# Performance work log

Hardware: AMD Instinct MI355X
Metric: run time of the kernel (lower is better)

Reference implementation:

```python
import jax, jax.numpy as jnp
import numpy as np

N_NODES = 100_000   # number of nodes
N_EDGES = 1_600_000 # number of edges (avg degree 16)
D_IN    = 64        # node feature dim
E_W     = 16        # edge feature ('w') dim -> message dim D_IN + E_W
EPS     = 0.0       # init_eps, non-learnable buffer


def setup_inputs() -> dict:
    key = jax.random.key(0)
    k1, k2, k3, k4, k5 = jax.random.split(key, 5)
    feat = jax.random.normal(k1, (N_NODES, D_IN), dtype=jnp.float32)
    edge_w = jax.random.normal(k2, (N_EDGES, E_W), dtype=jnp.float32)
    src = jax.random.randint(k3, (N_EDGES,), 0, N_NODES)
    dst = jax.random.randint(k4, (N_EDGES,), 0, N_NODES)
    # apply_func: Linear(D_IN + E_W -> D_IN)
    W = jax.random.normal(k5, (D_IN + E_W, D_IN), dtype=jnp.float32) / np.float32(np.sqrt(D_IN + E_W))
    b = jnp.zeros((D_IN,), dtype=jnp.float32)
    return {"feat": feat, "edge_w": edge_w, "W": W, "b": b, "src": src, "dst": dst}


def reference(feat, edge_w, W, b, src, dst):
    n = feat.shape[0]
    # message m_e = concat(h[src_e], w_e); sum-aggregate over incoming edges of dst.
    # Sum of concat == concat of sums, avoiding materializing [E, D_IN+E_W].
    neigh_h = jax.ops.segment_sum(feat[src], dst, num_segments=n)     # [N, D_IN]
    neigh_w = jax.ops.segment_sum(edge_w, dst, num_segments=n)        # [N, E_W]
    neigh = jnp.concatenate([neigh_h, neigh_w], axis=-1)              # [N, D_IN+E_W]
    # pad feat with zeros to match widened message dim (as in the torch code)
    feat_pad = jnp.concatenate(
        [feat, jnp.zeros((n, neigh.shape[-1] - feat.shape[-1]), feat.dtype)], axis=-1
    )
    rst = (1.0 + EPS) * feat_pad + neigh                              # eps-residual
    rst = rst @ W + b                                                 # apply_func (Linear)
    return jax.nn.relu(rst)                                           # activation
```

## Files before the change

kernel.cpp:

```cpp
#include <hip/hip_runtime.h>

#define D_IN  64
#define E_W   16
#define D_MSG 80
#define NXCD  8

static __device__ __forceinline__ void f4add(float4& a, const float4& b) {
    a.x += b.x; a.y += b.y; a.z += b.z; a.w += b.w;
}

__global__ __launch_bounds__(256) void k_hist_sh(const int4* __restrict__ dst4,
                                                 const int* __restrict__ dst,
                                                 int* __restrict__ deg,
                                                 int E, int rng)
{
    int shard = blockIdx.x & (NXCD - 1);
    int wg    = blockIdx.x / NXCD;
    int lo    = shard * rng;
    int hi    = lo + rng;
    int E4    = E >> 2;

    int base = wg * 512;
    int stop = min(base + 512, E4);
    for (int i = base + threadIdx.x; i < stop; i += 256) {
        int4 d = dst4[i];
        if (d.x >= lo && d.x < hi) atomicAdd(deg + d.x, 1);
        if (d.y >= lo && d.y < hi) atomicAdd(deg + d.y, 1);
        if (d.z >= lo && d.z < hi) atomicAdd(deg + d.z, 1);
        if (d.w >= lo && d.w < hi) atomicAdd(deg + d.w, 1);
    }
    if (wg == 0 && threadIdx.x < (E & 3)) {
        int e = (E & ~3) + threadIdx.x;
        int d = dst[e];
        if (d >= lo && d < hi) atomicAdd(deg + d, 1);
    }
}

__global__ __launch_bounds__(256) void k_scan1(const int* __restrict__ deg,
                                               int* __restrict__ excl,
                                               int* __restrict__ bsums, int n)
{
    __shared__ int ts[256];
    int base = blockIdx.x * 1024 + threadIdx.x * 4;
    int v[4], s = 0;
    #pragma unroll
    for (int i = 0; i < 4; ++i) { v[i] = (base + i < n) ? deg[base + i] : 0; s += v[i]; }
    ts[threadIdx.x] = s; __syncthreads();
    #pragma unroll
    for (int off = 1; off < 256; off <<= 1) {
        int t = (threadIdx.x >= off) ? ts[threadIdx.x - off] : 0;
        __syncthreads();
        ts[threadIdx.x] += t;
        __syncthreads();
    }
    int run = ts[threadIdx.x] - s;
    if (threadIdx.x == 255) bsums[blockIdx.x] = ts[255];
    #pragma unroll
    for (int i = 0; i < 4; ++i) {
        if (base + i < n) excl[base + i] = run;
        run += v[i];
    }
}

__global__ __launch_bounds__(256) void k_scan2(int* __restrict__ bsums,
                                               int* __restrict__ bexcl, int nb)
{
    __shared__ int ts[256];
    int v = (threadIdx.x < nb) ? bsums[threadIdx.x] : 0;
    ts[threadIdx.x] = v; __syncthreads();
    #pragma unroll
    for (int off = 1; off < 256; off <<= 1) {
        int t = (threadIdx.x >= off) ? ts[threadIdx.x - off] : 0;
        __syncthreads();
        ts[threadIdx.x] += t;
        __syncthreads();
    }
    bexcl[threadIdx.x] = ts[threadIdx.x] - v;
}

__global__ __launch_bounds__(256) void k_scan3(const int* __restrict__ excl,
                                               const int* __restrict__ bexcl,
                                               int* __restrict__ offsets,
                                               int* __restrict__ cursor, int n, int E)
{
    int i = blockIdx.x * 256 + threadIdx.x;
    if (i < n) {
        int s = excl[i] + bexcl[i >> 10];
        offsets[i] = s;
        cursor[i]  = s;
    }
    if (i == 0) offsets[n] = E;
}

__global__ __launch_bounds__(256) void k_reorder_sh(const int4* __restrict__ src4,
                                                    const int4* __restrict__ dst4,
                                                    const int* __restrict__ src,
                                                    const int* __restrict__ dst,
                                                    int* __restrict__ cursor,
                                                    int2* __restrict__ sorted,
                                                    int E, int rng)
{
    int shard = blockIdx.x & (NXCD - 1);
    int wg    = blockIdx.x / NXCD;
    int lo    = shard * rng;
    int hi    = lo + rng;
    int E4    = E >> 2;

    int base = wg * 512;
    int stop = min(base + 512, E4);
    for (int i = base + threadIdx.x; i < stop; i += 256) {
        int4 d = dst4[i];
        bool any = (d.x >= lo && d.x < hi) | (d.y >= lo && d.y < hi) |
                   (d.z >= lo && d.z < hi) | (d.w >= lo && d.w < hi);
        if (!any) continue;
        int4 s = src4[i];
        int e = i * 4;
        if (d.x >= lo && d.x < hi) sorted[atomicAdd(cursor + d.x, 1)] = make_int2(s.x, e + 0);
        if (d.y >= lo && d.y < hi) sorted[atomicAdd(cursor + d.y, 1)] = make_int2(s.y, e + 1);
        if (d.z >= lo && d.z < hi) sorted[atomicAdd(cursor + d.z, 1)] = make_int2(s.z, e + 2);
        if (d.w >= lo && d.w < hi) sorted[atomicAdd(cursor + d.w, 1)] = make_int2(s.w, e + 3);
    }
    if (wg == 0 && threadIdx.x < (E & 3)) {
        int e = (E & ~3) + threadIdx.x;
        int d = dst[e];
        if (d >= lo && d < hi) sorted[atomicAdd(cursor + d, 1)] = make_int2(src[e], e);
    }
}

__global__ __launch_bounds__(256) void k_pull(const float4* __restrict__ feat4,
                                              const float4* __restrict__ ew4,
                                              const int2* __restrict__ sorted,
                                              const int* __restrict__ offsets,
                                              float4* __restrict__ acc_h4,
                                              float4* __restrict__ acc_w4, int N)
{
    int t = blockIdx.x * 256 + threadIdx.x;
    int node = t >> 4;
    if (node >= N) return;
    int l = t & 15;

    int beg = offsets[node];
    int end = offsets[node + 1];

    float4 ah = feat4[(size_t)node * 16 + l];
    float4 aw = make_float4(0.f, 0.f, 0.f, 0.f);

    int p = beg;
    for (; p + 4 <= end; p += 4) {
        int2 r0 = sorted[p + 0];
        int2 r1 = sorted[p + 1];
        int2 r2 = sorted[p + 2];
        int2 r3 = sorted[p + 3];
        float4 f0 = feat4[(size_t)r0.x * 16 + l];
        float4 f1 = feat4[(size_t)r1.x * 16 + l];
        float4 f2 = feat4[(size_t)r2.x * 16 + l];
        float4 f3 = feat4[(size_t)r3.x * 16 + l];
        if (l < 4) {
            float4 w0 = ew4[(size_t)r0.y * 4 + l];
            float4 w1 = ew4[(size_t)r1.y * 4 + l];
            float4 w2 = ew4[(size_t)r2.y * 4 + l];
            float4 w3 = ew4[(size_t)r3.y * 4 + l];
            f4add(aw, w0); f4add(aw, w1); f4add(aw, w2); f4add(aw, w3);
        }
        f4add(ah, f0); f4add(ah, f1); f4add(ah, f2); f4add(ah, f3);
    }
    for (; p < end; ++p) {
        int2 r = sorted[p];
        f4add(ah, feat4[(size_t)r.x * 16 + l]);
        if (l < 4) f4add(aw, ew4[(size_t)r.y * 4 + l]);
    }

    acc_h4[(size_t)node * 16 + l] = ah;
    if (l < 4) acc_w4[(size_t)node * 4 + l] = aw;
}

__global__ __launch_bounds__(256) void scatter_kernel(
    const float4* __restrict__ feat4, const float4* __restrict__ ew4,
    const int* __restrict__ src, const int* __restrict__ dst,
    float* __restrict__ acc_h, float* __restrict__ acc_w, int E)
{
    int t = blockIdx.x * 256 + threadIdx.x;
    int e = t >> 4;
    if (e >= E) return;
    int l = t & 15;
    int s = src[e];
    int d = dst[e];
    float4 hv = feat4[(size_t)s * 16 + l];
    float4 wv;
    bool do_w = (l < 4);
    if (do_w) wv = ew4[(size_t)e * 4 + l];
    float* p = acc_h + (size_t)d * D_IN + l * 4;
    unsafeAtomicAdd(p + 0, hv.x);
    unsafeAtomicAdd(p + 1, hv.y);
    unsafeAtomicAdd(p + 2, hv.z);
    unsafeAtomicAdd(p + 3, hv.w);
    if (do_w) {
        float* q = acc_w + (size_t)d * E_W + l * 4;
        unsafeAtomicAdd(q + 0, wv.x);
        unsafeAtomicAdd(q + 1, wv.y);
        unsafeAtomicAdd(q + 2, wv.z);
        unsafeAtomicAdd(q + 3, wv.w);
    }
}

__global__ __launch_bounds__(256) void gemm_relu_kernel(
    const float* __restrict__ feat, const float* __restrict__ acc_w,
    const float* __restrict__ Wm, const float* __restrict__ bias,
    float* __restrict__ out, int N, int add_feat)
{
    __shared__ float4 Wl[D_MSG * 16];
    __shared__ float4 bl4[16];
    __shared__ float  xs[64 * 84];

    for (int i = threadIdx.x; i < D_MSG * 16; i += 256)
        Wl[i] = ((const float4*)Wm)[i];
    if (threadIdx.x < 16)
        bl4[threadIdx.x] = ((const float4*)bias)[threadIdx.x];

    const int tc   = threadIdx.x & 15;
    const int tg   = threadIdx.x >> 4;
    const int base = blockIdx.x * 64;

    for (int i = threadIdx.x; i < 64 * 20; i += 256) {
        int r = i / 20, c = i % 20;
        int row = base + r;
        float4 v = make_float4(0.f, 0.f, 0.f, 0.f);
        if (row < N) {
            if (c < 16) {
                v = ((const float4*)out)[(size_t)row * 16 + c];
                if (add_feat) {
                    float4 f = ((const float4*)feat)[(size_t)row * 16 + c];
                    f4add(v, f);
                }
            } else {
                v = ((const float4*)acc_w)[(size_t)row * 4 + (c - 16)];
            }
        }
        *((float4*)&xs[r * 84 + c * 4]) = v;
    }
    __syncthreads();

    float4 ob = bl4[tc];
    float4 acc[4];
    acc[0] = ob; acc[1] = ob; acc[2] = ob; acc[3] = ob;

    #pragma unroll 4
    for (int k = 0; k < D_MSG; ++k) {
        float4 w = Wl[k * 16 + tc];
        #pragma unroll
        for (int rr = 0; rr < 4; ++rr) {
            float xk = xs[(tg * 4 + rr) * 84 + k];
            acc[rr].x += xk * w.x;
            acc[rr].y += xk * w.y;
            acc[rr].z += xk * w.z;
            acc[rr].w += xk * w.w;
        }
    }

    #pragma unroll
    for (int rr = 0; rr < 4; ++rr) {
        int row = base + tg * 4 + rr;
        if (row < N) {
            float4 v = acc[rr];
            v.x = fmaxf(v.x, 0.f);
            v.y = fmaxf(v.y, 0.f);
            v.z = fmaxf(v.z, 0.f);
            v.w = fmaxf(v.w, 0.f);
            ((float4*)out)[(size_t)row * 16 + tc] = v;
        }
    }
}

static inline size_t align256(size_t x) { return (x + 255) & ~(size_t)255; }

extern "C" void kernel_launch(void* const* d_in, const int* in_sizes, int n_in,
                              void* d_out, int out_size, void* d_ws, size_t ws_size,
                              hipStream_t stream) {
    const float* feat   = (const float*)d_in[0];
    const float* edge_w = (const float*)d_in[1];
    const float* Wm     = (const float*)d_in[2];
    const float* bias   = (const float*)d_in[3];
    const int*   src    = (const int*)d_in[4];
    const int*   dst    = (const int*)d_in[5];
    float* out = (float*)d_out;

    const int N = in_sizes[0] / D_IN;
    const int E = in_sizes[4];

    size_t o_accw   = 0;
    size_t o_deg    = align256(o_accw + (size_t)N * E_W * 4);
    size_t o_excl   = align256(o_deg  + (size_t)(N + 1) * 4);
    size_t o_off    = align256(o_excl + (size_t)N * 4);
    size_t o_cur    = align256(o_off  + (size_t)(N + 1) * 4);
    size_t o_bsum   = align256(o_cur  + (size_t)N * 4);
    size_t o_bexcl  = align256(o_bsum + 256 * 4);
    size_t o_sorted = align256(o_bexcl + 256 * 4);
    size_t need     = o_sorted + (size_t)E * 8;

    char* ws = (char*)d_ws;
    float* acc_w = (float*)(ws + o_accw);

    int used_fallback = 0;

    if (ws_size >= need) {
        int*  deg     = (int*) (ws + o_deg);
        int*  excl    = (int*) (ws + o_excl);
        int*  offsets = (int*) (ws + o_off);
        int*  cursor  = (int*) (ws + o_cur);
        int*  bsums   = (int*) (ws + o_bsum);
        int*  bexcl   = (int*) (ws + o_bexcl);
        int2* sorted  = (int2*)(ws + o_sorted);

        hipMemsetAsync(deg, 0, (size_t)(N + 1) * 4, stream);

        const int rng = (N + NXCD - 1) / NXCD;
        const int E4  = E >> 2;
        const int wg_per_shard = (E4 + 511) / 512;
        const int grid_sh = wg_per_shard * NXCD;

        k_hist_sh<<<grid_sh, 256, 0, stream>>>((const int4*)dst, dst, deg, E, rng);

        int nb1 = (N + 1023) / 1024;
        k_scan1<<<nb1, 256, 0, stream>>>(deg, excl, bsums, N);
        k_scan2<<<1, 256, 0, stream>>>(bsums, bexcl, nb1);
        k_scan3<<<(N + 255) / 256, 256, 0, stream>>>(excl, bexcl, offsets, cursor, N, E);

        k_reorder_sh<<<grid_sh, 256, 0, stream>>>(
            (const int4*)src, (const int4*)dst, src, dst, cursor, sorted, E, rng);

        k_pull<<<(N * 16 + 255) / 256, 256, 0, stream>>>(
            (const float4*)feat, (const float4*)edge_w, sorted, offsets,
            (float4*)out, (float4*)acc_w, N);
    } else {
        used_fallback = 1;
        hipMemsetAsync(d_out, 0, (size_t)N * D_IN * sizeof(float), stream);
        hipMemsetAsync(acc_w, 0, (size_t)N * E_W * sizeof(float), stream);
        long long tot = (long long)E * 16;
        scatter_kernel<<<(int)((tot + 255) / 256), 256, 0, stream>>>(
            (const float4*)feat, (const float4*)edge_w, src, dst, out, acc_w, E);
    }

    gemm_relu_kernel<<<(N + 63) / 64, 256, 0, stream>>>(
        feat, acc_w, Wm, bias, out, N, used_fallback);
}
```

Measured before the change: 417.4 us.

## Fuse pull aggregation with linear+ReLU and collapse scan into one kernel

Each block now aggregates neighbor features for 16 nodes into shared memory, then applies the 80x64 linear layer, bias and ReLU directly. This drops the separate GEMM kernel and the round trip of aggregated rows through global memory. The three-kernel prefix scan becomes a single 1024-thread block that scans 100K degrees serially per thread, which cuts launches but leaves that step on one CU. Every block also reloads W (20KB) into LDS, which adds load traffic and LDS pressure.

```diff
diff --git a/kernel.cpp b/kernel.cpp
--- a/kernel.cpp
+++ b/kernel.cpp
@@ -36,60 +36,35 @@
     }
 }
 
-__global__ __launch_bounds__(256) void k_scan1(const int* __restrict__ deg,
-                                               int* __restrict__ excl,
-                                               int* __restrict__ bsums, int n)
-{
-    __shared__ int ts[256];
-    int base = blockIdx.x * 1024 + threadIdx.x * 4;
-    int v[4], s = 0;
+__global__ __launch_bounds__(1024) void k_scan_one(const int* __restrict__ deg,
+                                                   int* __restrict__ offsets,
+                                                   int* __restrict__ cursor,
+                                                   int n, int E)
+{
+    __shared__ int ts[1024];
+    const int C = (n + 1023) / 1024;
+    int t  = threadIdx.x;
+    int lo = t * C;
+    int hi = min(lo + C, n);
+
+    int s = 0;
+    for (int i = lo; i < hi; ++i) s += deg[i];
+    ts[t] = s; __syncthreads();
     #pragma unroll
-    for (int i = 0; i < 4; ++i) { v[i] = (base + i < n) ? deg[base + i] : 0; s += v[i]; }
-    ts[threadIdx.x] = s; __syncthreads();
-    #pragma unroll
-    for (int off = 1; off < 256; off <<= 1) {
-        int t = (threadIdx.x >= off) ? ts[threadIdx.x - off] : 0;
+    for (int off = 1; off < 1024; off <<= 1) {
+        int v = (t >= off) ? ts[t - off] : 0;
         __syncthreads();
-        ts[threadIdx.x] += t;
+        ts[t] += v;
         __syncthreads();
     }
-    int run = ts[threadIdx.x] - s;
-    if (threadIdx.x == 255) bsums[blockIdx.x] = ts[255];
-    #pragma unroll
-    for (int i = 0; i < 4; ++i) {
-        if (base + i < n) excl[base + i] = run;
-        run += v[i];
-    }
-}
-
-__global__ __launch_bounds__(256) void k_scan2(int* __restrict__ bsums,
-                                               int* __restrict__ bexcl, int nb)
-{
-    __shared__ int ts[256];
-    int v = (threadIdx.x < nb) ? bsums[threadIdx.x] : 0;
-    ts[threadIdx.x] = v; __syncthreads();
-    #pragma unroll
-    for (int off = 1; off < 256; off <<= 1) {
-        int t = (threadIdx.x >= off) ? ts[threadIdx.x - off] : 0;
-        __syncthreads();
-        ts[threadIdx.x] += t;
-        __syncthreads();
-    }
-    bexcl[threadIdx.x] = ts[threadIdx.x] - v;
-}
-
-__global__ __launch_bounds__(256) void k_scan3(const int* __restrict__ excl,
-                                               const int* __restrict__ bexcl,
-                                               int* __restrict__ offsets,
-                                               int* __restrict__ cursor, int n, int E)
-{
-    int i = blockIdx.x * 256 + threadIdx.x;
-    if (i < n) {
-        int s = excl[i] + bexcl[i >> 10];
-        offsets[i] = s;
-        cursor[i]  = s;
-    }
-    if (i == 0) offsets[n] = E;
+    int run = ts[t] - s;
+    for (int i = lo; i < hi; ++i) {
+        int d = deg[i];
+        offsets[i] = run;
+        cursor[i]  = run;
+        run += d;
+    }
+    if (t == 0) offsets[n] = E;
 }
 
 __global__ __launch_bounds__(256) void k_reorder_sh(const int4* __restrict__ src4,
@@ -127,51 +102,81 @@
     }
 }
 
-__global__ __launch_bounds__(256) void k_pull(const float4* __restrict__ feat4,
-                                              const float4* __restrict__ ew4,
-                                              const int2* __restrict__ sorted,
-                                              const int* __restrict__ offsets,
-                                              float4* __restrict__ acc_h4,
-                                              float4* __restrict__ acc_w4, int N)
-{
-    int t = blockIdx.x * 256 + threadIdx.x;
-    int node = t >> 4;
-    if (node >= N) return;
-    int l = t & 15;
-
-    int beg = offsets[node];
-    int end = offsets[node + 1];
-
-    float4 ah = feat4[(size_t)node * 16 + l];
-    float4 aw = make_float4(0.f, 0.f, 0.f, 0.f);
-
-    int p = beg;
-    for (; p + 4 <= end; p += 4) {
-        int2 r0 = sorted[p + 0];
-        int2 r1 = sorted[p + 1];
-        int2 r2 = sorted[p + 2];
-        int2 r3 = sorted[p + 3];
-        float4 f0 = feat4[(size_t)r0.x * 16 + l];
-        float4 f1 = feat4[(size_t)r1.x * 16 + l];
-        float4 f2 = feat4[(size_t)r2.x * 16 + l];
-        float4 f3 = feat4[(size_t)r3.x * 16 + l];
-        if (l < 4) {
-            float4 w0 = ew4[(size_t)r0.y * 4 + l];
-            float4 w1 = ew4[(size_t)r1.y * 4 + l];
-            float4 w2 = ew4[(size_t)r2.y * 4 + l];
-            float4 w3 = ew4[(size_t)r3.y * 4 + l];
-            f4add(aw, w0); f4add(aw, w1); f4add(aw, w2); f4add(aw, w3);
-        }
-        f4add(ah, f0); f4add(ah, f1); f4add(ah, f2); f4add(ah, f3);
-    }
-    for (; p < end; ++p) {
-        int2 r = sorted[p];
-        f4add(ah, feat4[(size_t)r.x * 16 + l]);
-        if (l < 4) f4add(aw, ew4[(size_t)r.y * 4 + l]);
-    }
-
-    acc_h4[(size_t)node * 16 + l] = ah;
-    if (l < 4) acc_w4[(size_t)node * 4 + l] = aw;
+__global__ __launch_bounds__(256) void k_pull_gemm(const float4* __restrict__ feat4,
+                                                   const float4* __restrict__ ew4,
+                                                   const int2* __restrict__ sorted,
+                                                   const int* __restrict__ offsets,
+                                                   const float* __restrict__ Wm,
+                                                   const float* __restrict__ bias,
+                                                   float4* __restrict__ out4, int N)
+{
+    __shared__ float4 Wl[D_MSG * 16];
+    __shared__ float4 bl4[16];
+    __shared__ float  xs[16 * 84];
+
+    for (int i = threadIdx.x; i < D_MSG * 16; i += 256)
+        Wl[i] = ((const float4*)Wm)[i];
+    if (threadIdx.x < 16)
+        bl4[threadIdx.x] = ((const float4*)bias)[threadIdx.x];
+
+    const int nl   = threadIdx.x >> 4;
+    const int l    = threadIdx.x & 15;
+    const int node = blockIdx.x * 16 + nl;
+
+    if (node < N) {
+        int beg = offsets[node];
+        int end = offsets[node + 1];
+
+        float4 ah = feat4[(size_t)node * 16 + l];
+        float4 aw = make_float4(0.f, 0.f, 0.f, 0.f);
+
+        int p = beg;
+        for (; p + 4 <= end; p += 4) {
+            int2 r0 = sorted[p + 0];
+            int2 r1 = sorted[p + 1];
+            int2 r2 = sorted[p + 2];
+            int2 r3 = sorted[p + 3];
+            float4 f0 = feat4[(size_t)r0.x * 16 + l];
+            float4 f1 = feat4[(size_t)r1.x * 16 + l];
+            float4 f2 = feat4[(size_t)r2.x * 16 + l];
+            float4 f3 = feat4[(size_t)r3.x * 16 + l];
+            if (l < 4) {
+                float4 w0 = ew4[(size_t)r0.y * 4 + l];
+                float4 w1 = ew4[(size_t)r1.y * 4 + l];
+                float4 w2 = ew4[(size_t)r2.y * 4 + l];
+                float4 w3 = ew4[(size_t)r3.y * 4 + l];
+                f4add(aw, w0); f4add(aw, w1); f4add(aw, w2); f4add(aw, w3);
+            }
+            f4add(ah, f0); f4add(ah, f1); f4add(ah, f2); f4add(ah, f3);
+        }
+        for (; p < end; ++p) {
+            int2 r = sorted[p];
+            f4add(ah, feat4[(size_t)r.x * 16 + l]);
+            if (l < 4) f4add(aw, ew4[(size_t)r.y * 4 + l]);
+        }
+
+        *(float4*)&xs[nl * 84 + l * 4] = ah;
+        if (l < 4) *(float4*)&xs[nl * 84 + 64 + l * 4] = aw;
+    }
+    __syncthreads();
+
+    if (node < N) {
+        float4 acc = bl4[l];
+        #pragma unroll 8
+        for (int k = 0; k < D_MSG; ++k) {
+            float  xk = xs[nl * 84 + k];
+            float4 w  = Wl[k * 16 + l];
+            acc.x += xk * w.x;
+            acc.y += xk * w.y;
+            acc.z += xk * w.z;
+            acc.w += xk * w.w;
+        }
+        acc.x = fmaxf(acc.x, 0.f);
+        acc.y = fmaxf(acc.y, 0.f);
+        acc.z = fmaxf(acc.z, 0.f);
+        acc.w = fmaxf(acc.w, 0.f);
+        out4[(size_t)node * 16 + l] = acc;
+    }
 }
 
 __global__ __launch_bounds__(256) void scatter_kernel(
@@ -300,15 +305,10 @@
     char* ws = (char*)d_ws;
     float* acc_w = (float*)(ws + o_accw);
 
-    int used_fallback = 0;
-
     if (ws_size >= need) {
         int*  deg     = (int*) (ws + o_deg);
-        int*  excl    = (int*) (ws + o_excl);
         int*  offsets = (int*) (ws + o_off);
         int*  cursor  = (int*) (ws + o_cur);
-        int*  bsums   = (int*) (ws + o_bsum);
-        int*  bexcl   = (int*) (ws + o_bexcl);
         int2* sorted  = (int2*)(ws + o_sorted);
 
         hipMemsetAsync(deg, 0, (size_t)(N + 1) * 4, stream);
@@ -320,26 +320,21 @@
 
         k_hist_sh<<<grid_sh, 256, 0, stream>>>((const int4*)dst, dst, deg, E, rng);
 
-        int nb1 = (N + 1023) / 1024;
-        k_scan1<<<nb1, 256, 0, stream>>>(deg, excl, bsums, N);
-        k_scan2<<<1, 256, 0, stream>>>(bsums, bexcl, nb1);
-        k_scan3<<<(N + 255) / 256, 256, 0, stream>>>(excl, bexcl, offsets, cursor, N, E);
+        k_scan_one<<<1, 1024, 0, stream>>>(deg, offsets, cursor, N, E);
 
         k_reorder_sh<<<grid_sh, 256, 0, stream>>>(
             (const int4*)src, (const int4*)dst, src, dst, cursor, sorted, E, rng);
 
-        k_pull<<<(N * 16 + 255) / 256, 256, 0, stream>>>(
+        k_pull_gemm<<<(N + 15) / 16, 256, 0, stream>>>(
             (const float4*)feat, (const float4*)edge_w, sorted, offsets,
-            (float4*)out, (float4*)acc_w, N);
+            Wm, bias, (float4*)out, N);
     } else {
-        used_fallback = 1;
         hipMemsetAsync(d_out, 0, (size_t)N * D_IN * sizeof(float), stream);
         hipMemsetAsync(acc_w, 0, (size_t)N * E_W * sizeof(float), stream);
         long long tot = (long long)E * 16;
         scatter_kernel<<<(int)((tot + 255) / 256), 256, 0, stream>>>(
             (const float4*)feat, (const float4*)edge_w, src, dst, out, acc_w, E);
-    }
-
-    gemm_relu_kernel<<<(N + 63) / 64, 256, 0, stream>>>(
-        feat, acc_w, Wm, bias, out, N, used_fallback);
-}
+        gemm_relu_kernel<<<(N + 63) / 64, 256, 0, stream>>>(
+            feat, acc_w, Wm, bias, out, N, 1);
+    }
+}
```

Result: slower. 627.3 us (+50.3%).
